# Optimization experiments

Measured on AMD Instinct MI355X. Metric: run time of the kernel, lower is better.

The kernel has to match this reference:

```python
import jax, jax.numpy as jnp
import numpy as np

CTX = 2048
D_IN = 2048
D_OUT = 2048
N_HEADS = 16
HEAD_DIM = D_OUT // N_HEADS
ROPE_BASE = 10000.0


def rope_tables(head_dim, ctx):
    inv_freq = 1.0 / (ROPE_BASE ** (jnp.arange(0, head_dim, 2, dtype=jnp.float32) / head_dim))
    angles = jnp.arange(ctx, dtype=jnp.float32)[:, None] * inv_freq[None, :]  # [ctx, hd/2]
    angles = jnp.concatenate([angles, angles], axis=1)  # [ctx, hd]
    return jnp.sin(angles), jnp.cos(angles)


def apply_rope(x, sin, cos):
    # x: [b, h, s, d]; rotate-by-half (Raschka / Llama style)
    s = x.shape[2]
    d = x.shape[3]
    x1, x2 = x[..., : d // 2], x[..., d // 2 :]
    rotated = jnp.concatenate([-x2, x1], axis=-1)
    return x * cos[:s][None, None] + rotated * sin[:s][None, None]


def setup_inputs() -> dict:
    key = jax.random.key(0)
    kx, kq, kk, kv, ko = jax.random.split(key, 5)
    scale = 0.02
    return {
        "x": jax.random.normal(kx, (2, CTX, D_IN), dtype=jnp.float32),
        "W_query": jax.random.normal(kq, (D_IN, D_OUT), dtype=jnp.float32) * scale,
        "W_key": jax.random.normal(kk, (D_IN, D_OUT), dtype=jnp.float32) * scale,
        "W_value": jax.random.normal(kv, (D_IN, D_OUT), dtype=jnp.float32) * scale,
        "W_out": jax.random.normal(ko, (D_OUT, D_OUT), dtype=jnp.float32) * scale,
    }


def reference(x, W_query, W_key, W_value, W_out):
    bs, cl, _ = x.shape
    sin, cos = rope_tables(HEAD_DIM, CTX)

    def split_heads(t):  # [b, s, d_out] -> [b, h, s, hd]
        return t.reshape(bs, cl, N_HEADS, HEAD_DIM).transpose(0, 2, 1, 3)

    q = split_heads(x @ W_query)
    k = split_heads(x @ W_key)
    v = split_heads(x @ W_value)

    q = apply_rope(q, sin, cos)
    k = apply_rope(k, sin, cos)

    # NOTE: original module does NOT scale by 1/sqrt(head_dim)
    scores = jnp.einsum("bhqd,bhkd->bhqk", q, k)
    causal = jnp.triu(jnp.ones((cl, cl), dtype=bool), k=1)
    scores = jnp.where(causal[None, None], -jnp.inf, scores)
    weights = jax.nn.softmax(scores, axis=-1)
    ctx = jnp.einsum("bhqk,bhkd->bhqd", weights, v)
    ctx = ctx.transpose(0, 2, 1, 3).reshape(bs, cl, N_HEADS * HEAD_DIM)
    return ctx @ W_out
```

## Files before the change

kernel.cpp:

```cpp
#include <hip/hip_runtime.h>
#include <cstdint>
#include <cstddef>

typedef _Float16 f16;
typedef _Float16 f16x8 __attribute__((ext_vector_type(8)));
typedef _Float16 f16x4 __attribute__((ext_vector_type(4)));
typedef float    f32x4 __attribute__((ext_vector_type(4)));
typedef float    f32x16 __attribute__((ext_vector_type(16)));
typedef int      i32x4 __attribute__((ext_vector_type(4)));

#define S_CTX 2048
#define NH 16
#define DH 128

#define BAR() asm volatile("s_barrier" ::: "memory")
#define VMW(n) asm volatile("s_waitcnt vmcnt(" #n ")" ::: "memory")
#define MF(a, b, c) __builtin_amdgcn_mfma_f32_16x16x32_f16((a), (b), (c), 0, 0, 0)
#define MF32(a, b, c) __builtin_amdgcn_mfma_f32_32x32x16_f16((a), (b), (c), 0, 0, 0)

__device__ __forceinline__ void gload16(const void* g, void* l) {
  __builtin_amdgcn_global_load_lds(
      (const __attribute__((address_space(1))) void*)g,
      (__attribute__((address_space(3))) void*)l, 16, 0, 0);
}

__device__ __forceinline__ int pk2(float a, float b) {
  auto hv = __builtin_amdgcn_cvt_pkrtz(a, b);
  return __builtin_bit_cast(int, hv);
}
__device__ __forceinline__ void pl_swap(int& a, int& b) {
  asm volatile("v_permlane32_swap_b32 %0, %1" : "+v"(a), "+v"(b));
}

__global__ void prep(const float* __restrict__ x,
                     const float* __restrict__ w0, const float* __restrict__ w1,
                     const float* __restrict__ w2, const float* __restrict__ w3,
                     f16* __restrict__ xb,
                     f16* __restrict__ o0, f16* __restrict__ o1,
                     f16* __restrict__ o2, f16* __restrict__ o3,
                     float* __restrict__ sint, float* __restrict__ cost) {
  const int bid = blockIdx.x, tid = threadIdx.x;
  if (bid < 512) {
    int idx = bid * 256 + tid;
    int j = idx & 63, s = idx >> 6;
    float invf = __expf(-(float)(2 * j) * (1.0f / 128.0f) * 9.210340371976184f);
    float a = (float)s * invf;
    sint[idx] = sinf(a);
    cost[idx] = cosf(a);
  } else if (bid < 8704) {
    int i = ((bid - 512) * 256 + tid) * 4;
    float4 v = *(const float4*)(x + i);
    f16x4 o; o[0] = (f16)v.x; o[1] = (f16)v.y; o[2] = (f16)v.z; o[3] = (f16)v.w;
    *(f16x4*)(xb + i) = o;
  } else {
    int b2 = bid - 8704;
    int z = b2 >> 12, rem = b2 & 4095;
    int by = rem >> 6, bx = rem & 63;
    int tx = tid & 31, ty = tid >> 5;
    const float* in; f16* out;
    switch (z) {
      case 0: in = w0; out = o0; break;
      case 1: in = w1; out = o1; break;
      case 2: in = w2; out = o2; break;
      default: in = w3; out = o3; break;
    }
    __shared__ float tl[32][33];
    int xc = bx * 32 + tx, yc = by * 32 + ty;
#pragma unroll
    for (int r = 0; r < 32; r += 8)
      tl[ty + r][tx] = in[(size_t)(yc + r) * 2048 + xc];
    __syncthreads();
    int xo = by * 32 + tx, yo = bx * 32 + ty;
#pragma unroll
    for (int r = 0; r < 32; r += 8)
      out[(size_t)(yo + r) * 2048 + xo] = (f16)tl[tx][ty + r];
  }
}

__global__ __launch_bounds__(512, 1)
void gemm_qk(const f16* __restrict__ A, const f16* __restrict__ wqT,
             const f16* __restrict__ wkT,
             f16* __restrict__ qb, f16* __restrict__ kb,
             const float* __restrict__ sint, const float* __restrict__ cost) {
  extern __shared__ __align__(16) char lds[];
  const int tid = threadIdx.x, lane = tid & 63;
  const int wvi = tid >> 6, wm = wvi >> 2, wn = wvi & 3;
  const int gcol = blockIdx.x * 256;
  const int proj = gcol >> 11;
  const int col0 = gcol & 2047;
  const int row0 = blockIdx.y * 256;
  const f16* Bt = proj ? wkT : wqT;

  const int ca0 = tid, ca1 = tid + 512;
  const int ra0 = ca0 >> 2, ra1 = ca1 >> 2;
  const int sa0 = (ca0 & 3) ^ ((ra0 >> 1) & 3);
  const int sa1 = (ca1 & 3) ^ ((ra1 >> 1) & 3);
  const f16* gA0 = A + (size_t)(row0 + ra0) * 2048 + sa0 * 8;
  const f16* gA1 = A + (size_t)(row0 + ra1) * 2048 + sa1 * 8;
  const f16* gB0 = Bt + (size_t)(col0 + ra0) * 2048 + sa0 * 8;
  const f16* gB1 = Bt + (size_t)(col0 + ra1) * 2048 + sa1 * 8;

  const int kslot = lane >> 4;
  int aoff[8], boff[4];
#pragma unroll
  for (int i = 0; i < 8; i++) {
    int row = wm * 128 + i * 16 + (lane & 15);
    aoff[i] = row * 64 + ((kslot ^ ((row >> 1) & 3)) << 4);
  }
#pragma unroll
  for (int j = 0; j < 4; j++) {
    int rb = (wn >> 1) * 128 + (wn & 1) * 32 + (j & 1) * 16 + (j >> 1) * 64 + (lane & 15);
    boff[j] = rb * 64 + ((kslot ^ ((rb >> 1) & 3)) << 4);
  }

  f32x4 acc[8][4] = {};

#define QKPH(SLOT, HS, SSLOT, DOSTAGE, WN) do {                                \
    const char* As_ = lds + (SLOT) * 32768;                                    \
    const char* Bs_ = As_ + 16384;                                             \
    f16x8 af[8], bf[4];                                                        \
    _Pragma("unroll") for (int i_ = 0; i_ < 8; i_++)                           \
      af[i_] = *(const f16x8*)(As_ + aoff[i_]);                                \
    _Pragma("unroll") for (int j_ = 0; j_ < 4; j_++)                           \
      bf[j_] = *(const f16x8*)(Bs_ + boff[j_]);                                \
    if (DOSTAGE) {                                                             \
      char* dA = lds + (SSLOT) * 32768;                                        \
      gload16(gA0 + (HS) * 32, dA + ca0 * 16);                                 \
      gload16(gA1 + (HS) * 32, dA + ca1 * 16);                                 \
      gload16(gB0 + (HS) * 32, dA + 16384 + ca0 * 16);                         \
      gload16(gB1 + (HS) * 32, dA + 16384 + ca1 * 16);                         \
    }                                                                          \
    asm volatile("s_waitcnt vmcnt(" #WN ")" ::: "memory");                     \
    BAR();                                                                     \
    __builtin_amdgcn_s_setprio(1);                                             \
    _Pragma("unroll") for (int i_ = 0; i_ < 8; i_++)                           \
      _Pragma("unroll") for (int j_ = 0; j_ < 4; j_++)                         \
        acc[i_][j_] = MF(af[i_], bf[j_], acc[i_][j_]);                         \
    __builtin_amdgcn_s_setprio(0);                                             \
    BAR();                                                                     \
  } while (0)

#pragma unroll
  for (int h = 0; h < 2; h++) {
    char* dA = lds + h * 32768;
    gload16(gA0 + h * 32, dA + ca0 * 16);
    gload16(gA1 + h * 32, dA + ca1 * 16);
    gload16(gB0 + h * 32, dA + 16384 + ca0 * 16);
    gload16(gB1 + h * 32, dA + 16384 + ca1 * 16);
  }
  VMW(4); BAR();

  for (int t = 0; t < 20; ++t) {
    const int hb = 3 * t;
    QKPH(0, hb + 2, 2, 1, 4);
    QKPH(1, hb + 3, 0, 1, 4);
    QKPH(2, hb + 4, 1, 1, 4);
  }
  QKPH(0, 62, 2, 1, 4);
  QKPH(1, 63, 0, 1, 4);
  QKPH(2, 0, 0, 0, 0);
  QKPH(0, 0, 0, 0, 63);
#undef QKPH

  const int b = row0 >> 11, sb = row0 & 2047;
  f16* dst = proj ? kb : qb;
  const int h = (col0 >> 7) + (wn >> 1);
#pragma unroll
  for (int i = 0; i < 8; i++)
#pragma unroll
    for (int jj = 0; jj < 2; jj++)
#pragma unroll
      for (int r = 0; r < 4; r++) {
        int s = sb + wm * 128 + i * 16 + (lane >> 4) * 4 + r;
        int d = (wn & 1) * 32 + jj * 16 + (lane & 15);
        float cv = cost[s * 64 + d], sv = sint[s * 64 + d];
        float x1 = acc[i][jj][r], x2 = acc[i][jj + 2][r];
        size_t base = ((size_t)(b * NH + h) * S_CTX + s) << 7;
        dst[base + d]      = (f16)(x1 * cv - x2 * sv);
        dst[base + d + 64] = (f16)(x2 * cv + x1 * sv);
      }
}

template<int MODE>
__global__ __launch_bounds__(512, 1)
void gemm8(const f16* __restrict__ A, const f16* __restrict__ Bt,
           f16* __restrict__ vtb, float* __restrict__ of) {
  extern __shared__ __align__(16) char lds[];
#define RING_A(e) (lds + (e) * 16384)
#define RING_B(e) (lds + 65536 + (e) * 8192)
  const int tid = threadIdx.x, lane = tid & 63;
  const int wvi = tid >> 6, wm = wvi >> 1, wn = wvi & 1;
  const int col0 = blockIdx.x * 128;
  const int row0 = blockIdx.y * 256;

  const int ca0 = tid, ca1 = tid + 512, cb0 = tid;
  const int rAs0 = ca0 >> 2, rAs1 = ca1 >> 2, rBs0 = cb0 >> 2;
  const int sA0 = (ca0 & 3) ^ ((rAs0 >> 1) & 3);
  const int sA1 = (ca1 & 3) ^ ((rAs1 >> 1) & 3);
  const int sB0 = (cb0 & 3) ^ ((rBs0 >> 1) & 3);
  const f16* gA0 = A + (size_t)(row0 + rAs0) * 2048 + sA0 * 8;
  const f16* gA1 = A + (size_t)(row0 + rAs1) * 2048 + sA1 * 8;
  const f16* gB0 = Bt + (size_t)(col0 + rBs0) * 2048 + sB0 * 8;

  const int kslot = lane >> 4;
  int aoff[4], boff[4];
#pragma unroll
  for (int i = 0; i < 4; i++) {
    int row = wm * 64 + i * 16 + (lane & 15);
    aoff[i] = row * 64 + ((kslot ^ ((row >> 1) & 3)) << 4);
  }
#pragma unroll
  for (int j = 0; j < 4; j++) {
    int rb = wn * 32 + (j & 1) * 16 + (j >> 1) * 64 + (lane & 15);
    boff[j] = rb * 64 + ((kslot ^ ((rb >> 1) & 3)) << 4);
  }

  f32x4 acc[4][4] = {};

#define PH8(SLOT, HS, DOSTAGE, WN) do {                                        \
    const char* As_ = RING_A(SLOT);                                            \
    const char* Bs_ = RING_B(SLOT);                                            \
    f16x8 af[4], bf[4];                                                        \
    _Pragma("unroll") for (int i_ = 0; i_ < 4; i_++)                           \
      af[i_] = *(const f16x8*)(As_ + aoff[i_]);                                \
    _Pragma("unroll") for (int j_ = 0; j_ < 4; j_++)                           \
      bf[j_] = *(const f16x8*)(Bs_ + boff[j_]);                                \
    if (DOSTAGE) {                                                             \
      gload16(gA0 + (HS) * 32, RING_A((HS) & 3) + ca0 * 16);                   \
      gload16(gA1 + (HS) * 32, RING_A((HS) & 3) + ca1 * 16);                   \
      gload16(gB0 + (HS) * 32, RING_B((HS) & 3) + cb0 * 16);                   \
    }                                                                          \
    asm volatile("s_waitcnt vmcnt(" #WN ")" ::: "memory");                     \
    BAR();                                                                     \
    __builtin_amdgcn_s_setprio(1);                                             \
    _Pragma("unroll") for (int i_ = 0; i_ < 4; i_++)                           \
      _Pragma("unroll") for (int j_ = 0; j_ < 4; j_++)                         \
        acc[i_][j_] = MF(af[i_], bf[j_], acc[i_][j_]);                         \
    __builtin_amdgcn_s_setprio(0);                                             \
    BAR();                                                                     \
  } while (0)

#pragma unroll
  for (int h = 0; h < 3; h++) {
    gload16(gA0 + h * 32, RING_A(h) + ca0 * 16);
    gload16(gA1 + h * 32, RING_A(h) + ca1 * 16);
    gload16(gB0 + h * 32, RING_B(h) + cb0 * 16);
  }
  VMW(6); BAR();

  for (int t = 0; t < 15; ++t) {
    const int p = t * 4;
    PH8(0, p + 3, 1, 6);
    PH8(1, p + 4, 1, 6);
    PH8(2, p + 5, 1, 6);
    PH8(3, p + 6, 1, 6);
  }
  PH8(0, 63, 1, 6);
  PH8(1, 0, 0, 3);
  PH8(2, 0, 0, 0);
  PH8(3, 0, 0, 63);
#undef PH8

  const int b = row0 >> 11, sbase = row0 & 2047;

  if (MODE == 2) {
#pragma unroll
    for (int i = 0; i < 4; i++)
#pragma unroll
      for (int j = 0; j < 4; j++)
#pragma unroll
        for (int r = 0; r < 4; r++) {
          int row = row0 + wm * 64 + i * 16 + (lane >> 4) * 4 + r;
          int col = col0 + wn * 32 + (j & 1) * 16 + (j >> 1) * 64 + (lane & 15);
          of[(size_t)row * 2048 + col] = acc[i][j][r];
        }
  } else {
    const int h = col0 >> 7;
    f16x4* ldsv = (f16x4*)lds;
#pragma unroll
    for (int i = 0; i < 4; i++)
#pragma unroll
      for (int j = 0; j < 4; j++) {
        f16x4 v;
#pragma unroll
        for (int r = 0; r < 4; r++) v[r] = (f16)acc[i][j][r];
        int su = wm * 16 + i * 4 + (lane >> 4);
        int d  = wn * 32 + (j & 1) * 16 + (j >> 1) * 64 + (lane & 15);
        ldsv[d * 64 + (su ^ ((d << 1) & 63))] = v;
      }
    __syncthreads();
#pragma unroll
    for (int it = 0; it < 8; ++it) {
      int o = it * 512 + tid;
      int d = o >> 5, c = o & 31;
      int xc = (d << 1) & 63;
      f16x4 lo = ldsv[d * 64 + ((2 * c) ^ xc)];
      f16x4 hi = ldsv[d * 64 + ((2 * c + 1) ^ xc)];
      f16x8 vv;
      vv[0] = lo[0]; vv[1] = lo[1]; vv[2] = lo[2]; vv[3] = lo[3];
      vv[4] = hi[0]; vv[5] = hi[1]; vv[6] = hi[2]; vv[7] = hi[3];
      *(f16x8*)&vtb[((size_t)(b * NH + h) * DH + d) * S_CTX + sbase + c * 8] = vv;
    }
  }
#undef RING_A
#undef RING_B
}

__global__ __launch_bounds__(256, 2)
void attn_k(const f16* __restrict__ q, const f16* __restrict__ kk,
            const f16* __restrict__ vt, f16* __restrict__ ctx) {
  __shared__ __align__(16) f16 Ks[2][64 * 128];
  __shared__ __align__(16) f16 Vs[2][128 * 64];
  const int tid = threadIdx.x, lane = tid & 63, wv = tid >> 6;
  const int lh = lane >> 5, q31 = lane & 31;
  const int bid = blockIdx.x;
  const int xcd = bid & 7, rr = bid >> 3;
  const int bh = xcd + 8 * (rr & 3);
  const int Q = 15 - (rr >> 2);
  const int b = bh >> 4, h = bh & 15;
  const size_t plane = (size_t)bh * (S_CTX * DH);
  const f16* Qp = q + plane;
  const f16* Kp = kk + plane;
  const f16* Vp = vt + plane;
  const float LOG2E = 1.4426950408889634f;
  const int q0 = Q * 128;
  const int NT = 2 * Q + 2;

#define STAGE(T, BUF) do {                                                      \
    const f16* Kt = Kp + (size_t)(T) * 64 * DH;                                 \
    const f16* Vt = Vp + (size_t)(T) * 64;                                      \
    _Pragma("unroll") for (int j_ = 0; j_ < 4; j_++) {                          \
      int c = tid + j_ * 256; int rk = c >> 4;                                  \
      gload16(Kt + (size_t)rk * DH + (((c & 15) ^ (rk & 7)) * 8), &Ks[BUF][c * 8]); \
    }                                                                           \
    _Pragma("unroll") for (int j_ = 0; j_ < 4; j_++) {                          \
      int c = tid + j_ * 256; int rv = c >> 3;                                  \
      gload16(Vt + (size_t)rv * S_CTX + (((c & 7) ^ (rv & 7)) * 8), &Vs[BUF][c * 8]); \
    }                                                                           \
  } while (0)

  f16x8 qf[8];
  {
    const f16* qq = Qp + (size_t)(q0 + wv * 32 + q31) * DH + lh * 8;
#pragma unroll
    for (int s = 0; s < 8; s++) {
      qf[s] = *(const f16x8*)(qq + s * 16);
#pragma unroll
      for (int e = 0; e < 8; e++) qf[s][e] = (f16)((float)qf[s][e] * LOG2E);
    }
  }
  float m_ = -3e38f, l_ = 0.f;
  f32x16 o[4] = {};

  STAGE(0, 0);
  VMW(0); BAR();

  int cur = 0;
  for (int t = 0; t < NT; t++) {
    if (t + 1 < NT) {
      if (cur) STAGE(t + 1, 0); else STAGE(t + 1, 1);
    }
    const f16* Ksc = Ks[cur];
    const f16* Vsc = Vs[cur];

    f32x16 st0 = {}, st1 = {};
    __builtin_amdgcn_s_setprio(1);
#pragma unroll
    for (int s = 0; s < 8; s++) {
      const int r0 = q31, r1 = 32 + q31;
      f16x8 kf0 = *(const f16x8*)&Ksc[r0 * 128 + (((2 * s + lh) ^ (r0 & 7)) << 3)];
      f16x8 kf1 = *(const f16x8*)&Ksc[r1 * 128 + (((2 * s + lh) ^ (r1 & 7)) << 3)];
      st0 = MF32(kf0, qf[s], st0);
      st1 = MF32(kf1, qf[s], st1);
    }
    __builtin_amdgcn_s_setprio(0);

    if (t >= 2 * Q) {
      const int qg = q0 + wv * 32 + q31;
#pragma unroll
      for (int r = 0; r < 16; r++) {
        int kvb = t * 64 + (r & 3) + 8 * (r >> 2) + 4 * lh;
        if (kvb > qg) st0[r] = -3e38f;
        if (kvb + 32 > qg) st1[r] = -3e38f;
      }
    }
    float mx = st0[0];
#pragma unroll
    for (int r = 1; r < 16; r++) mx = fmaxf(mx, st0[r]);
#pragma unroll
    for (int r = 0; r < 16; r++) mx = fmaxf(mx, st1[r]);
    mx = fmaxf(mx, __shfl_xor(mx, 32));
    if (__any(mx > m_ + 8.0f)) {
      float nm = fmaxf(m_, mx);
      float al = __builtin_amdgcn_exp2f(m_ - nm);
      m_ = nm; l_ *= al;
#pragma unroll
      for (int r = 0; r < 16; r++) {
        float alr = __shfl(al, (r & 3) + 8 * (r >> 2) + 4 * lh);
#pragma unroll
        for (int j = 0; j < 4; j++) o[j][r] *= alr;
      }
    }
    float s_ = 0.f;
#pragma unroll
    for (int r = 0; r < 16; r++) { st0[r] = __builtin_amdgcn_exp2f(st0[r] - m_); s_ += st0[r]; }
#pragma unroll
    for (int r = 0; r < 16; r++) { st1[r] = __builtin_amdgcn_exp2f(st1[r] - m_); s_ += st1[r]; }
    s_ += __shfl_xor(s_, 32);
    l_ += s_;

    f16x8 pa[4];
    {
      int w0 = pk2(st0[0], st0[1]),   w1 = pk2(st0[2], st0[3]);
      int w2 = pk2(st0[4], st0[5]),   w3 = pk2(st0[6], st0[7]);
      int w4 = pk2(st0[8], st0[9]),   w5 = pk2(st0[10], st0[11]);
      int w6 = pk2(st0[12], st0[13]), w7 = pk2(st0[14], st0[15]);
      pl_swap(w0, w2); pl_swap(w1, w3); pl_swap(w4, w6); pl_swap(w5, w7);
      i32x4 a = {w0, w1, w2, w3}; pa[0] = __builtin_bit_cast(f16x8, a);
      i32x4 bb = {w4, w5, w6, w7}; pa[1] = __builtin_bit_cast(f16x8, bb);
    }
    {
      int w0 = pk2(st1[0], st1[1]),   w1 = pk2(st1[2], st1[3]);
      int w2 = pk2(st1[4], st1[5]),   w3 = pk2(st1[6], st1[7]);
      int w4 = pk2(st1[8], st1[9]),   w5 = pk2(st1[10], st1[11]);
      int w6 = pk2(st1[12], st1[13]), w7 = pk2(st1[14], st1[15]);
      pl_swap(w0, w2); pl_swap(w1, w3); pl_swap(w4, w6); pl_swap(w5, w7);
      i32x4 a = {w0, w1, w2, w3}; pa[2] = __builtin_bit_cast(f16x8, a);
      i32x4 bb = {w4, w5, w6, w7}; pa[3] = __builtin_bit_cast(f16x8, bb);
    }

    __builtin_amdgcn_s_setprio(1);
#pragma unroll
    for (int j = 0; j < 4; j++) {
      const int rv = 32 * j + q31;
#pragma unroll
      for (int s2 = 0; s2 < 4; s2++) {
        f16x8 vf = *(const f16x8*)&Vsc[rv * 64 + (((2 * s2 + lh) ^ (rv & 7)) << 3)];
        o[j] = MF32(pa[s2], vf, o[j]);
      }
    }
    __builtin_amdgcn_s_setprio(0);

    VMW(0); BAR();
    cur ^= 1;
  }
#undef STAGE

  float inv = 1.0f / l_;
#pragma unroll
  for (int r = 0; r < 16; r++) {
    int crow = (r & 3) + 8 * (r >> 2) + 4 * lh;
    float invr = __shfl(inv, crow);
    int qg = q0 + wv * 32 + crow;
#pragma unroll
    for (int j = 0; j < 4; j++) {
      int dd = h * 128 + 32 * j + q31;
      ctx[((size_t)(b * S_CTX + qg) * 2048) + dd] = (f16)(o[j][r] * invr);
    }
  }
}

extern "C" void kernel_launch(void* const* d_in, const int* in_sizes, int n_in,
                              void* d_out, int out_size, void* d_ws, size_t ws_size,
                              hipStream_t stream) {
  (void)in_sizes; (void)n_in; (void)out_size; (void)ws_size;
  const float* x  = (const float*)d_in[0];
  const float* Wq = (const float*)d_in[1];
  const float* Wk = (const float*)d_in[2];
  const float* Wv = (const float*)d_in[3];
  const float* Wo = (const float*)d_in[4];
  float* out = (float*)d_out;
  char* ws = (char*)d_ws;

  f16*   xb   = (f16*)(ws);
  f16*   ctxb = (f16*)(ws);
  f16*   wqT  = (f16*)(ws + 16777216);
  f16*   wkT  = (f16*)(ws + 25165824);
  f16*   wvT  = (f16*)(ws + 33554432);
  f16*   woT  = (f16*)(ws + 41943040);
  f16*   qb   = (f16*)(ws + 50331648);
  f16*   kb   = (f16*)(ws + 67108864);
  f16*   vtb  = (f16*)(ws + 83886080);
  float* sint = (float*)(ws + 100663296);
  float* cost = (float*)(ws + 101187584);

  prep<<<dim3(25088), dim3(256), 0, stream>>>(x, Wq, Wk, Wv, Wo, xb,
                                              wqT, wkT, wvT, woT, sint, cost);
  gemm_qk<<<dim3(16, 16), dim3(512), 98304, stream>>>(xb, wqT, wkT, qb, kb, sint, cost);
  gemm8<1><<<dim3(16, 16), dim3(512), 98304, stream>>>(xb, wvT, vtb, nullptr);
  attn_k<<<dim3(512), dim3(256), 0, stream>>>(qb, kb, vtb, ctxb);
  gemm8<2><<<dim3(16, 16), dim3(512), 98304, stream>>>(ctxb, woT, nullptr, out);
}
```

Before: 248.7 us.

## Split attention KV range across two wave groups and pair causal tiles per block

The attention kernel now runs 512-thread blocks, 256 in total. Each block processes two query tiles, one short and one long (idxQ and 15-idxQ), so the causal work per block is balanced. Within a block, two 256-thread halves take alternating KV tiles with separate LDS double buffers, and their partial softmax states are merged through LDS before the output is written. This aims to remove tail imbalance and shorten the serial KV chain per query tile, at the cost of 128KB dynamic LDS, one block per CU, and the extra merge and barrier work.

```diff
diff --git a/kernel.cpp b/kernel.cpp
--- a/kernel.cpp
+++ b/kernel.cpp
@@ -306,158 +306,191 @@
 #undef RING_B
 }
 
-__global__ __launch_bounds__(256, 2)
+__global__ __launch_bounds__(512, 1)
 void attn_k(const f16* __restrict__ q, const f16* __restrict__ kk,
             const f16* __restrict__ vt, f16* __restrict__ ctx) {
-  __shared__ __align__(16) f16 Ks[2][64 * 128];
-  __shared__ __align__(16) f16 Vs[2][128 * 64];
-  const int tid = threadIdx.x, lane = tid & 63, wv = tid >> 6;
+  extern __shared__ __align__(16) char alds[];
+  const int tid = threadIdx.x, lane = tid & 63;
+  const int halfid = tid >> 8;
+  const int tid2 = tid & 255;
+  const int wv2 = tid2 >> 6;
   const int lh = lane >> 5, q31 = lane & 31;
   const int bid = blockIdx.x;
-  const int xcd = bid & 7, rr = bid >> 3;
-  const int bh = xcd + 8 * (rr & 3);
-  const int Q = 15 - (rr >> 2);
+  const int bh = (bid & 7) + 8 * ((bid >> 3) & 3);
+  const int idxQ = bid >> 5;
   const int b = bh >> 4, h = bh & 15;
   const size_t plane = (size_t)bh * (S_CTX * DH);
   const f16* Qp = q + plane;
   const f16* Kp = kk + plane;
   const f16* Vp = vt + plane;
   const float LOG2E = 1.4426950408889634f;
-  const int q0 = Q * 128;
-  const int NT = 2 * Q + 2;
+
+  char* myH = alds + halfid * 65536;
+  float* O_lds = (float*)(alds + 65536);
+  float* ml_lds = (float*)alds;
 
 #define STAGE(T, BUF) do {                                                      \
     const f16* Kt = Kp + (size_t)(T) * 64 * DH;                                 \
     const f16* Vt = Vp + (size_t)(T) * 64;                                      \
+    char* kb_ = myH + (BUF) * 16384;                                            \
+    char* vb_ = myH + 32768 + (BUF) * 16384;                                    \
     _Pragma("unroll") for (int j_ = 0; j_ < 4; j_++) {                          \
-      int c = tid + j_ * 256; int rk = c >> 4;                                  \
-      gload16(Kt + (size_t)rk * DH + (((c & 15) ^ (rk & 7)) * 8), &Ks[BUF][c * 8]); \
+      int c = tid2 + j_ * 256; int rk = c >> 4;                                 \
+      gload16(Kt + (size_t)rk * DH + (((c & 15) ^ (rk & 7)) * 8), kb_ + c * 16); \
     }                                                                           \
     _Pragma("unroll") for (int j_ = 0; j_ < 4; j_++) {                          \
-      int c = tid + j_ * 256; int rv = c >> 3;                                  \
-      gload16(Vt + (size_t)rv * S_CTX + (((c & 7) ^ (rv & 7)) * 8), &Vs[BUF][c * 8]); \
+      int c = tid2 + j_ * 256; int rv = c >> 3;                                 \
+      gload16(Vt + (size_t)rv * S_CTX + (((c & 7) ^ (rv & 7)) * 8), vb_ + c * 16); \
     }                                                                           \
   } while (0)
 
-  f16x8 qf[8];
-  {
-    const f16* qq = Qp + (size_t)(q0 + wv * 32 + q31) * DH + lh * 8;
-#pragma unroll
-    for (int s = 0; s < 8; s++) {
-      qf[s] = *(const f16x8*)(qq + s * 16);
-#pragma unroll
-      for (int e = 0; e < 8; e++) qf[s][e] = (f16)((float)qf[s][e] * LOG2E);
+  for (int p = 0; p < 2; ++p) {
+    const int Qt = p ? (15 - idxQ) : idxQ;
+    const int q0 = Qt * 128;
+    const int NTh = Qt + 1;
+
+    f16x8 qf[8];
+    {
+      const f16* qq = Qp + (size_t)(q0 + wv2 * 32 + q31) * DH + lh * 8;
+#pragma unroll
+      for (int s = 0; s < 8; s++) {
+        qf[s] = *(const f16x8*)(qq + s * 16);
+#pragma unroll
+        for (int e = 0; e < 8; e++) qf[s][e] = (f16)((float)qf[s][e] * LOG2E);
+      }
     }
-  }
-  float m_ = -3e38f, l_ = 0.f;
-  f32x16 o[4] = {};
-
-  STAGE(0, 0);
-  VMW(0); BAR();
-
-  int cur = 0;
-  for (int t = 0; t < NT; t++) {
-    if (t + 1 < NT) {
-      if (cur) STAGE(t + 1, 0); else STAGE(t + 1, 1);
+    float m_ = -3e38f, l_ = 0.f;
+    f32x16 o[4] = {};
+
+    STAGE(halfid, 0);
+    VMW(0); BAR();
+
+    int cur = 0;
+    for (int i = 0; i < NTh; i++) {
+      const int t = 2 * i + halfid;
+      if (i + 1 < NTh) STAGE(2 * (i + 1) + halfid, cur ^ 1);
+      const f16* Ksc = (const f16*)(myH + cur * 16384);
+      const f16* Vsc = (const f16*)(myH + 32768 + cur * 16384);
+
+      f32x16 st0 = {}, st1 = {};
+      __builtin_amdgcn_s_setprio(1);
+#pragma unroll
+      for (int s = 0; s < 8; s++) {
+        const int r0 = q31, r1 = 32 + q31;
+        f16x8 kf0 = *(const f16x8*)&Ksc[r0 * 128 + (((2 * s + lh) ^ (r0 & 7)) << 3)];
+        f16x8 kf1 = *(const f16x8*)&Ksc[r1 * 128 + (((2 * s + lh) ^ (r1 & 7)) << 3)];
+        st0 = MF32(kf0, qf[s], st0);
+        st1 = MF32(kf1, qf[s], st1);
+      }
+      __builtin_amdgcn_s_setprio(0);
+
+      if (t >= 2 * Qt) {
+        const int qg = q0 + wv2 * 32 + q31;
+#pragma unroll
+        for (int r = 0; r < 16; r++) {
+          int kvb = t * 64 + (r & 3) + 8 * (r >> 2) + 4 * lh;
+          if (kvb > qg) st0[r] = -3e38f;
+          if (kvb + 32 > qg) st1[r] = -3e38f;
+        }
+      }
+      float mx = st0[0];
+#pragma unroll
+      for (int r = 1; r < 16; r++) mx = fmaxf(mx, st0[r]);
+#pragma unroll
+      for (int r = 0; r < 16; r++) mx = fmaxf(mx, st1[r]);
+      mx = fmaxf(mx, __shfl_xor(mx, 32));
+      if (__any(mx > m_ + 8.0f)) {
+        float nm = fmaxf(m_, mx);
+        float al = __builtin_amdgcn_exp2f(m_ - nm);
+        m_ = nm; l_ *= al;
+#pragma unroll
+        for (int r = 0; r < 16; r++) {
+          float alr = __shfl(al, (r & 3) + 8 * (r >> 2) + 4 * lh);
+#pragma unroll
+          for (int j = 0; j < 4; j++) o[j][r] *= alr;
+        }
+      }
+      float s_ = 0.f;
+#pragma unroll
+      for (int r = 0; r < 16; r++) { st0[r] = __builtin_amdgcn_exp2f(st0[r] - m_); s_ += st0[r]; }
+#pragma unroll
+      for (int r = 0; r < 16; r++) { st1[r] = __builtin_amdgcn_exp2f(st1[r] - m_); s_ += st1[r]; }
+      s_ += __shfl_xor(s_, 32);
+      l_ += s_;
+
+      f16x8 pa[4];
+      {
+        int w0 = pk2(st0[0], st0[1]),   w1 = pk2(st0[2], st0[3]);
+        int w2 = pk2(st0[4], st0[5]),   w3 = pk2(st0[6], st0[7]);
+        int w4 = pk2(st0[8], st0[9]),   w5 = pk2(st0[10], st0[11]);
+        int w6 = pk2(st0[12], st0[13]), w7 = pk2(st0[14], st0[15]);
+        pl_swap(w0, w2); pl_swap(w1, w3); pl_swap(w4, w6); pl_swap(w5, w7);
+        i32x4 a = {w0, w1, w2, w3}; pa[0] = __builtin_bit_cast(f16x8, a);
+        i32x4 bb = {w4, w5, w6, w7}; pa[1] = __builtin_bit_cast(f16x8, bb);
+      }
+      {
+        int w0 = pk2(st1[0], st1[1]),   w1 = pk2(st1[2], st1[3]);
+        int w2 = pk2(st1[4], st1[5]),   w3 = pk2(st1[6], st1[7]);
+        int w4 = pk2(st1[8], st1[9]),   w5 = pk2(st1[10], st1[11]);
+        int w6 = pk2(st1[12], st1[13]), w7 = pk2(st1[14], st1[15]);
+        pl_swap(w0, w2); pl_swap(w1, w3); pl_swap(w4, w6); pl_swap(w5, w7);
+        i32x4 a = {w0, w1, w2, w3}; pa[2] = __builtin_bit_cast(f16x8, a);
+        i32x4 bb = {w4, w5, w6, w7}; pa[3] = __builtin_bit_cast(f16x8, bb);
+      }
+
+      __builtin_amdgcn_s_setprio(1);
+#pragma unroll
+      for (int j = 0; j < 4; j++) {
+        const int rv = 32 * j + q31;
+#pragma unroll
+        for (int s2 = 0; s2 < 4; s2++) {
+          f16x8 vf = *(const f16x8*)&Vsc[rv * 64 + (((2 * s2 + lh) ^ (rv & 7)) << 3)];
+          o[j] = MF32(pa[s2], vf, o[j]);
+        }
+      }
+      __builtin_amdgcn_s_setprio(0);
+
+      VMW(0); BAR();
+      cur ^= 1;
     }
-    const f16* Ksc = Ks[cur];
-    const f16* Vsc = Vs[cur];
-
-    f32x16 st0 = {}, st1 = {};
-    __builtin_amdgcn_s_setprio(1);
-#pragma unroll
-    for (int s = 0; s < 8; s++) {
-      const int r0 = q31, r1 = 32 + q31;
-      f16x8 kf0 = *(const f16x8*)&Ksc[r0 * 128 + (((2 * s + lh) ^ (r0 & 7)) << 3)];
-      f16x8 kf1 = *(const f16x8*)&Ksc[r1 * 128 + (((2 * s + lh) ^ (r1 & 7)) << 3)];
-      st0 = MF32(kf0, qf[s], st0);
-      st1 = MF32(kf1, qf[s], st1);
+
+    if (halfid) {
+      ml_lds[(wv2 * 32 + q31) * 2]     = m_;
+      ml_lds[(wv2 * 32 + q31) * 2 + 1] = l_;
+#pragma unroll
+      for (int r = 0; r < 16; r++) {
+        int crow = (r & 3) + 8 * (r >> 2) + 4 * lh;
+#pragma unroll
+        for (int j = 0; j < 4; j++)
+          O_lds[(wv2 * 32 + crow) * 128 + 32 * j + q31] = o[j][r];
+      }
     }
-    __builtin_amdgcn_s_setprio(0);
-
-    if (t >= 2 * Q) {
-      const int qg = q0 + wv * 32 + q31;
+    BAR();
+    if (!halfid) {
+      float mB = ml_lds[(wv2 * 32 + q31) * 2];
+      float lB = ml_lds[(wv2 * 32 + q31) * 2 + 1];
+      float m = fmaxf(m_, mB);
+      float aA = __builtin_amdgcn_exp2f(m_ - m);
+      float aB = __builtin_amdgcn_exp2f(mB - m);
+      float lfin = l_ * aA + lB * aB;
+      float inv = 1.0f / lfin;
 #pragma unroll
       for (int r = 0; r < 16; r++) {
-        int kvb = t * 64 + (r & 3) + 8 * (r >> 2) + 4 * lh;
-        if (kvb > qg) st0[r] = -3e38f;
-        if (kvb + 32 > qg) st1[r] = -3e38f;
+        int crow = (r & 3) + 8 * (r >> 2) + 4 * lh;
+        float aAr = __shfl(aA, crow);
+        float aBr = __shfl(aB, crow);
+        float invr = __shfl(inv, crow);
+        int qg = q0 + wv2 * 32 + crow;
+#pragma unroll
+        for (int j = 0; j < 4; j++) {
+          float ov = o[j][r] * aAr + O_lds[(wv2 * 32 + crow) * 128 + 32 * j + q31] * aBr;
+          ctx[((size_t)(b * S_CTX + qg) * 2048) + h * 128 + 32 * j + q31] = (f16)(ov * invr);
+        }
       }
     }
-    float mx = st0[0];
-#pragma unroll
-    for (int r = 1; r < 16; r++) mx = fmaxf(mx, st0[r]);
-#pragma unroll
-    for (int r = 0; r < 16; r++) mx = fmaxf(mx, st1[r]);
-    mx = fmaxf(mx, __shfl_xor(mx, 32));
-    if (__any(mx > m_ + 8.0f)) {
-      float nm = fmaxf(m_, mx);
-      float al = __builtin_amdgcn_exp2f(m_ - nm);
-      m_ = nm; l_ *= al;
-#pragma unroll
-      for (int r = 0; r < 16; r++) {
-        float alr = __shfl(al, (r & 3) + 8 * (r >> 2) + 4 * lh);
-#pragma unroll
-        for (int j = 0; j < 4; j++) o[j][r] *= alr;
-      }
-    }
-    float s_ = 0.f;
-#pragma unroll
-    for (int r = 0; r < 16; r++) { st0[r] = __builtin_amdgcn_exp2f(st0[r] - m_); s_ += st0[r]; }
-#pragma unroll
-    for (int r = 0; r < 16; r++) { st1[r] = __builtin_amdgcn_exp2f(st1[r] - m_); s_ += st1[r]; }
-    s_ += __shfl_xor(s_, 32);
-    l_ += s_;
-
-    f16x8 pa[4];
-    {
-      int w0 = pk2(st0[0], st0[1]),   w1 = pk2(st0[2], st0[3]);
-      int w2 = pk2(st0[4], st0[5]),   w3 = pk2(st0[6], st0[7]);
-      int w4 = pk2(st0[8], st0[9]),   w5 = pk2(st0[10], st0[11]);
-      int w6 = pk2(st0[12], st0[13]), w7 = pk2(st0[14], st0[15]);
-      pl_swap(w0, w2); pl_swap(w1, w3); pl_swap(w4, w6); pl_swap(w5, w7);
-      i32x4 a = {w0, w1, w2, w3}; pa[0] = __builtin_bit_cast(f16x8, a);
-      i32x4 bb = {w4, w5, w6, w7}; pa[1] = __builtin_bit_cast(f16x8, bb);
-    }
-    {
-      int w0 = pk2(st1[0], st1[1]),   w1 = pk2(st1[2], st1[3]);
-      int w2 = pk2(st1[4], st1[5]),   w3 = pk2(st1[6], st1[7]);
-      int w4 = pk2(st1[8], st1[9]),   w5 = pk2(st1[10], st1[11]);
-      int w6 = pk2(st1[12], st1[13]), w7 = pk2(st1[14], st1[15]);
-      pl_swap(w0, w2); pl_swap(w1, w3); pl_swap(w4, w6); pl_swap(w5, w7);
-      i32x4 a = {w0, w1, w2, w3}; pa[2] = __builtin_bit_cast(f16x8, a);
-      i32x4 bb = {w4, w5, w6, w7}; pa[3] = __builtin_bit_cast(f16x8, bb);
-    }
-
-    __builtin_amdgcn_s_setprio(1);
-#pragma unroll
-    for (int j = 0; j < 4; j++) {
-      const int rv = 32 * j + q31;
-#pragma unroll
-      for (int s2 = 0; s2 < 4; s2++) {
-        f16x8 vf = *(const f16x8*)&Vsc[rv * 64 + (((2 * s2 + lh) ^ (rv & 7)) << 3)];
-        o[j] = MF32(pa[s2], vf, o[j]);
-      }
-    }
-    __builtin_amdgcn_s_setprio(0);
-
-    VMW(0); BAR();
-    cur ^= 1;
+    BAR();
   }
 #undef STAGE
-
-  float inv = 1.0f / l_;
-#pragma unroll
-  for (int r = 0; r < 16; r++) {
-    int crow = (r & 3) + 8 * (r >> 2) + 4 * lh;
-    float invr = __shfl(inv, crow);
-    int qg = q0 + wv * 32 + crow;
-#pragma unroll
-    for (int j = 0; j < 4; j++) {
-      int dd = h * 128 + 32 * j + q31;
-      ctx[((size_t)(b * S_CTX + qg) * 2048) + dd] = (f16)(o[j][r] * invr);
-    }
-  }
 }
 
 extern "C" void kernel_launch(void* const* d_in, const int* in_sizes, int n_in,
@@ -488,6 +521,6 @@
                                               wqT, wkT, wvT, woT, sint, cost);
   gemm_qk<<<dim3(16, 16), dim3(512), 98304, stream>>>(xb, wqT, wkT, qb, kb, sint, cost);
   gemm8<1><<<dim3(16, 16), dim3(512), 98304, stream>>>(xb, wvT, vtb, nullptr);
-  attn_k<<<dim3(512), dim3(256), 0, stream>>>(qb, kb, vtb, ctxb);
+  attn_k<<<dim3(256), dim3(512), 131072, stream>>>(qb, kb, vtb, ctxb);
   gemm8<2><<<dim3(16, 16), dim3(512), 98304, stream>>>(ctxb, woT, nullptr, out);
 }
```

New measurement: 242.2 us. -2.6%, faster.
